# Optimization experiments

Hardware: AMD Instinct MI355X
Metric: run time of the kernel (lower is better)

The kernel has to match this reference:

```python
import jax, jax.numpy as jnp
import numpy as np
from jax import lax


def _conv1x1(x, w):
    # x: [B,Cin,H,W], w: [Cout,Cin]
    return jnp.einsum('bchw,oc->bohw', x, w)


def _dwconv(x, w, pad):
    # depthwise conv, w: [C,1,k,k]
    return lax.conv_general_dilated(
        x, w, window_strides=(1, 1), padding=[(pad, pad), (pad, pad)],
        dimension_numbers=('NCHW', 'OIHW', 'NCHW'),
        feature_group_count=w.shape[0])


def _l2norm(x, axis=-1, eps=1e-12):
    n = jnp.sqrt(jnp.sum(x * x, axis=axis, keepdims=True))
    return x / jnp.maximum(n, eps)


def _topk_masked_softmax(attn, k):
    # attn: [B,H,C,C]; keep top-k per row, -inf elsewhere, softmax
    B, H, C, _ = attn.shape
    flat = attn.reshape(B * H * C, C)
    vals, idx = lax.top_k(flat, k)
    rows = jnp.arange(flat.shape[0])[:, None]
    scat = jnp.full_like(flat, -jnp.inf).at[rows, idx].set(vals)
    return jax.nn.softmax(scat, axis=-1).reshape(B, H, C, C)


def setup_inputs() -> dict:
    key = jax.random.key(0)
    ks = jax.random.split(key, 7)
    dim, heads = 384, 8
    x = jax.random.normal(ks[0], (2, dim, 128, 128), jnp.float32)
    s = 0.02
    w_qkv = jax.random.normal(ks[1], (dim * 3, dim), jnp.float32) * s
    w_dw3 = jax.random.normal(ks[2], (dim * 3, 1, 3, 3), jnp.float32) * s
    w_dw5 = jax.random.normal(ks[3], (dim * 3, 1, 5, 5), jnp.float32) * s
    w_dw7 = jax.random.normal(ks[4], (dim * 3, 1, 7, 7), jnp.float32) * s
    w_pconv = jax.random.normal(ks[5], (dim * 3, dim * 9), jnp.float32) * s
    w_proj = jax.random.normal(ks[6], (dim, dim), jnp.float32) * s
    temperature = jnp.ones((heads, 1, 1), jnp.float32)
    attn_scales = jnp.full((3,), 0.2, jnp.float32)
    return {"x": x, "w_qkv": w_qkv, "w_dw3": w_dw3, "w_dw5": w_dw5,
            "w_dw7": w_dw7, "w_pconv": w_pconv, "w_proj": w_proj,
            "temperature": temperature, "attn_scales": attn_scales}


def reference(x, w_qkv, w_dw3, w_dw5, w_dw7, w_pconv, w_proj, temperature, attn_scales):
    b, c, h, w = x.shape
    heads = temperature.shape[0]
    base = _conv1x1(x, w_qkv)                       # [B,3C,H,W]
    qkv = jnp.concatenate([_dwconv(base, w_dw3, 1),
                           _dwconv(base, w_dw5, 2),
                           _dwconv(base, w_dw7, 3)], axis=1)  # [B,9C,H,W]
    qkv = _conv1x1(qkv, w_pconv)                    # [B,3C,H,W]
    q, k, v = jnp.split(qkv, 3, axis=1)
    def heads_split(t):
        return t.reshape(b, heads, c // heads, h * w)
    q, k, v = heads_split(q), heads_split(k), heads_split(v)
    q = _l2norm(q)
    k = _l2norm(k)
    attn = jnp.einsum('bhcn,bhdn->bhcd', q, k) * temperature  # [B,H,C,C]
    C = q.shape[2]
    out = jnp.zeros_like(v)
    for i, top_k in enumerate([int(C / 2), int(C * 2 / 3), int(C * 3 / 4)]):
        a = _topk_masked_softmax(attn, top_k)
        out = out + attn_scales[i] * jnp.einsum('bhcd,bhdn->bhcn', a, v)
    out = out.reshape(b, c, h, w)
    return _conv1x1(out, w_proj)
```

## Files before the change

kernel.cpp:

```cpp
#include <hip/hip_runtime.h>
#include <hip/hip_bf16.h>
#include <stdint.h>

typedef __attribute__((ext_vector_type(4))) float f32x4;
typedef __attribute__((ext_vector_type(8))) short s16x8;
typedef __attribute__((ext_vector_type(4))) short s16x4;
typedef __attribute__((ext_vector_type(8))) _Float16 f16x8;

__device__ __forceinline__ float bf2f(unsigned short u){
  union { unsigned int i; float f; } v; v.i = ((unsigned int)u) << 16; return v.f;
}
__device__ __forceinline__ unsigned short f2bf(float f){
  union { float f; unsigned int i; } v; v.f = f;
  unsigned int r = v.i + 0x7fffu + ((v.i >> 16) & 1u);
  return (unsigned short)(r >> 16);
}
__device__ __forceinline__ unsigned short f2h(float f){
  union { _Float16 h; unsigned short u; } v; v.h = (_Float16)f; return v.u;
}
__device__ __forceinline__ void gload_lds16(const void* g, void* l){
  __builtin_amdgcn_global_load_lds(
      (const __attribute__((address_space(1))) void*)g,
      (__attribute__((address_space(3))) void*)l, 16, 0, 0);
}

__device__ __forceinline__ void swz_decode(int id, int mtiles, int& m0, int& n0){
  const int xcd = id & 7;
  const int r = id >> 3;
  m0 = (r % mtiles) * 128;
  n0 = ((r / mtiles)*8 + xcd) * 128;
}

template<int MODE>
__global__ __launch_bounds__(256, 2)
void k_gemm(const unsigned short* __restrict__ A, const unsigned short* __restrict__ Bt,
            void* __restrict__ Cp, int M, int N, int K, int ldb){
  __shared__ unsigned short sm[16384];
  const int tid = threadIdx.x;
  const int lane = tid & 63;
  const int wid = tid >> 6;
  int m0, n0;
  swz_decode(blockIdx.x, M >> 7, m0, n0);
  const int wm = wid & 1;
  const int wn = wid >> 1;

  f32x4 acc[4][4];
  #pragma unroll
  for (int i = 0; i < 4; ++i)
    #pragma unroll
    for (int j = 0; j < 4; ++j)
      acc[i][j] = (f32x4){0.f, 0.f, 0.f, 0.f};

  const unsigned short* ga[4];
  const unsigned short* gb[4];
  unsigned short* la[4];
  unsigned short* lb[4];
  #pragma unroll
  for (int i = 0; i < 4; ++i){
    const int row = (wid*4 + i)*8 + (lane >> 3);
    const int slot = (lane & 7) ^ (row & 7);
    ga[i] = A  + (size_t)(m0 + row)*K   + slot*8;
    gb[i] = Bt + (size_t)(n0 + row)*ldb + slot*8;
    la[i] = &sm[(wid*4 + i)*512];
    lb[i] = &sm[8192 + (wid*4 + i)*512];
  }

  const int nkt = K >> 6;
  for (int kt = 0; kt < nkt; ++kt){
    if (kt) __syncthreads();
    #pragma unroll
    for (int i = 0; i < 4; ++i){
      gload_lds16(ga[i] + kt*64, la[i]);
      gload_lds16(gb[i] + kt*64, lb[i]);
    }
    __syncthreads();
    #pragma unroll
    for (int kk = 0; kk < 2; ++kk){
      s16x8 af[4], bfv[4];
      #pragma unroll
      for (int im = 0; im < 4; ++im){
        const int row = wm*64 + im*16 + (lane & 15);
        const int s = ((kk*4) | (lane >> 4)) ^ (row & 7);
        af[im] = *(const s16x8*)((const char*)sm + row*128 + s*16);
      }
      #pragma unroll
      for (int in = 0; in < 4; ++in){
        const int row = wn*64 + in*16 + (lane & 15);
        const int s = ((kk*4) | (lane >> 4)) ^ (row & 7);
        bfv[in] = *(const s16x8*)((const char*)sm + 16384 + row*128 + s*16);
      }
      #pragma unroll
      for (int im = 0; im < 4; ++im)
        #pragma unroll
        for (int in = 0; in < 4; ++in)
          acc[im][in] = __builtin_amdgcn_mfma_f32_16x16x32_bf16(af[im], bfv[in], acc[im][in], 0, 0, 0);
    }
  }

  float* C = (float*)Cp;
  #pragma unroll
  for (int im = 0; im < 4; ++im){
    const int m = m0 + wm*64 + im*16 + (lane >> 4)*4;
    #pragma unroll
    for (int in = 0; in < 4; ++in){
      const int n = n0 + wn*64 + in*16 + (lane & 15);
      #pragma unroll
      for (int r = 0; r < 4; ++r)
        C[(size_t)(m + r)*N + n] = acc[im][in][r];
    }
  }
}

__global__ __launch_bounds__(256, 3)
void k_gemm4w(const unsigned short* __restrict__ A, const unsigned short* __restrict__ Bt,
              float* __restrict__ C){
  __shared__ unsigned short sm[22528];
  const int tid = threadIdx.x;
  const int lane = tid & 63;
  const int wid = tid >> 6;
  const int xcd = blockIdx.x & 7;
  const int rr = blockIdx.x >> 3;
  const int m0 = (rr % 12) * 96;
  const int n0 = ((rr/12)*8 + xcd) * 256;
  const int wm = wid & 1;
  const int wn = wid >> 1;

  f32x4 acc[3][8];
  #pragma unroll
  for (int i = 0; i < 3; ++i)
    #pragma unroll
    for (int j = 0; j < 8; ++j)
      acc[i][j] = (f32x4){0.f, 0.f, 0.f, 0.f};

  const unsigned short* ga[3];
  unsigned short* la[3];
  const unsigned short* gb[8];
  unsigned short* lb[8];
  #pragma unroll
  for (int i = 0; i < 3; ++i){
    const int row = (wid*3 + i)*8 + (lane >> 3);
    const int slot = (lane & 7) ^ (row & 7);
    ga[i] = A + (size_t)(m0 + row)*1152 + slot*8;
    la[i] = &sm[(wid*3 + i)*512];
  }
  #pragma unroll
  for (int i = 0; i < 8; ++i){
    const int row = (wid*8 + i)*8 + (lane >> 3);
    const int slot = (lane & 7) ^ (row & 7);
    gb[i] = Bt + (size_t)(n0 + row)*1152 + slot*8;
    lb[i] = &sm[6144 + (wid*8 + i)*512];
  }

  for (int kt = 0; kt < 18; ++kt){
    if (kt) __syncthreads();
    #pragma unroll
    for (int i = 0; i < 3; ++i)
      gload_lds16(ga[i] + kt*64, la[i]);
    #pragma unroll
    for (int i = 0; i < 8; ++i)
      gload_lds16(gb[i] + kt*64, lb[i]);
    __syncthreads();
    #pragma unroll
    for (int kk = 0; kk < 2; ++kk){
      s16x8 af[3], bfv[8];
      #pragma unroll
      for (int im = 0; im < 3; ++im){
        const int row = wm*48 + im*16 + (lane & 15);
        const int s = ((kk*4) | (lane >> 4)) ^ (row & 7);
        af[im] = *(const s16x8*)((const char*)sm + row*128 + s*16);
      }
      #pragma unroll
      for (int in = 0; in < 8; ++in){
        const int row = wn*128 + in*16 + (lane & 15);
        const int s = ((kk*4) | (lane >> 4)) ^ (row & 7);
        bfv[in] = *(const s16x8*)((const char*)sm + 12288 + row*128 + s*16);
      }
      #pragma unroll
      for (int im = 0; im < 3; ++im)
        #pragma unroll
        for (int in = 0; in < 8; ++in)
          acc[im][in] = __builtin_amdgcn_mfma_f32_16x16x32_bf16(af[im], bfv[in], acc[im][in], 0, 0, 0);
    }
  }

  float* ep = (float*)sm;
  for (int p = 0; p < 4; ++p){
    __syncthreads();
    if (wn == (p >> 1)){
      #pragma unroll
      for (int in2 = 0; in2 < 4; ++in2){
        const int n2 = in2*16 + (lane & 15);
        const int e = (n2 & 7) << 2;
        #pragma unroll
        for (int im = 0; im < 3; ++im){
          const int t = (wm*48 + im*16 + (lane >> 4)*4) >> 2;
          *(f32x4*)(&ep[n2*128 + ((t ^ e) << 2)]) = acc[im][(p & 1)*4 + in2];
        }
      }
    }
    __syncthreads();
    #pragma unroll
    for (int j = 0; j < 6; ++j){
      const int cidx = tid + j*256;
      const int n2 = cidx / 24, t = cidx % 24;
      const int e = (n2 & 7) << 2;
      const f32x4 v = *(const f32x4*)(&ep[n2*128 + ((t ^ e) << 2)]);
      const int cb = (m0 >> 4) + (t >> 2);
      const int off = (t & 3)*4;
      float* dst = C + ((size_t)cb*16384 + (n0 + p*64 + n2))*16 + off;
      *(f32x4*)dst = v;
    }
  }
}

__global__ __launch_bounds__(256, 3)
void k_gemm_f9(const unsigned short* __restrict__ Wp16, const unsigned short* __restrict__ Bt,
               float* __restrict__ qkT, unsigned short* __restrict__ vT, int startPx, int cpx){
  __shared__ unsigned short sm[22528];
  const int tid = threadIdx.x;
  const int lane = tid & 63;
  const int wid = tid >> 6;
  const int xcd = blockIdx.x & 7;
  const int rr = blockIdx.x >> 3;
  const int m0 = (rr % 12) * 96;
  const int n0 = ((rr/12)*8 + xcd) * 256;
  const bool isV = (m0 >= 768);
  const int wm = wid & 1;
  const int wn = wid >> 1;

  f32x4 acc[3][8];
  #pragma unroll
  for (int i = 0; i < 3; ++i)
    #pragma unroll
    for (int j = 0; j < 8; ++j)
      acc[i][j] = (f32x4){0.f, 0.f, 0.f, 0.f};

  const unsigned short* ga[3];
  unsigned short* la[3];
  const unsigned short* gb[8];
  unsigned short* lb[8];
  #pragma unroll
  for (int i = 0; i < 3; ++i){
    const int row = (wid*3 + i)*8 + (lane >> 3);
    const int slot = (lane & 7) ^ (row & 7);
    ga[i] = Wp16 + (size_t)(m0 + row)*3456 + slot*8;
    la[i] = &sm[(wid*3 + i)*512];
  }
  #pragma unroll
  for (int i = 0; i < 8; ++i){
    const int row = (wid*8 + i)*8 + (lane >> 3);
    const int slot = (lane & 7) ^ (row & 7);
    gb[i] = Bt + (size_t)(n0 + row)*3456 + slot*8;
    lb[i] = &sm[6144 + (wid*8 + i)*512];
  }

  for (int kt = 0; kt < 54; ++kt){
    if (kt) __syncthreads();
    #pragma unroll
    for (int i = 0; i < 3; ++i)
      gload_lds16(ga[i] + kt*64, la[i]);
    #pragma unroll
    for (int i = 0; i < 8; ++i)
      gload_lds16(gb[i] + kt*64, lb[i]);
    __syncthreads();
    #pragma unroll
    for (int kk = 0; kk < 2; ++kk){
      f16x8 af[3], bfv[8];
      #pragma unroll
      for (int im = 0; im < 3; ++im){
        const int row = wm*48 + im*16 + (lane & 15);
        const int s = ((kk*4) | (lane >> 4)) ^ (row & 7);
        af[im] = *(const f16x8*)((const char*)sm + row*128 + s*16);
      }
      #pragma unroll
      for (int in = 0; in < 8; ++in){
        const int row = wn*128 + in*16 + (lane & 15);
        const int s = ((kk*4) | (lane >> 4)) ^ (row & 7);
        bfv[in] = *(const f16x8*)((const char*)sm + 12288 + row*128 + s*16);
      }
      #pragma unroll
      for (int im = 0; im < 3; ++im)
        #pragma unroll
        for (int in = 0; in < 8; ++in)
          acc[im][in] = __builtin_amdgcn_mfma_f32_16x16x32_f16(af[im], bfv[in], acc[im][in], 0, 0, 0);
    }
  }

  float* ep = (float*)sm;
  for (int p = 0; p < 4; ++p){
    __syncthreads();
    if (wn == (p >> 1)){
      #pragma unroll
      for (int in2 = 0; in2 < 4; ++in2){
        const int n2 = in2*16 + (lane & 15);
        const int e = (n2 & 7) << 2;
        #pragma unroll
        for (int im = 0; im < 3; ++im){
          const int t = (wm*48 + im*16 + (lane >> 4)*4) >> 2;
          *(f32x4*)(&ep[n2*128 + ((t ^ e) << 2)]) = acc[im][(p & 1)*4 + in2];
        }
      }
    }
    __syncthreads();
    if (!isV){
      #pragma unroll
      for (int j = 0; j < 6; ++j){
        const int cidx = tid + j*256;
        const int n2 = cidx / 24, t = cidx % 24;
        const int e = (n2 & 7) << 2;
        const f32x4 v = *(const f32x4*)(&ep[n2*128 + ((t ^ e) << 2)]);
        *(f32x4*)(qkT + (size_t)(n0 + p*64 + n2)*768 + m0 + t*4) = v;
      }
    } else {
      #pragma unroll
      for (int j = 0; j < 3; ++j){
        const int cidx = tid + j*256;
        const int n2 = cidx / 12, u2 = cidx % 12;
        const int e = (n2 & 7) << 2;
        const f32x4 lo = *(const f32x4*)(&ep[n2*128 + (((2*u2    ) ^ e) << 2)]);
        const f32x4 hi = *(const f32x4*)(&ep[n2*128 + (((2*u2 + 1) ^ e) << 2)]);
        s16x8 o;
        #pragma unroll
        for (int q = 0; q < 4; ++q){ o[q] = (short)f2bf(lo[q]); o[4 + q] = (short)f2bf(hi[q]); }
        *(s16x8*)(vT + (size_t)(startPx + n0 + p*64 + n2)*384 + (m0 - 768) + u2*8) = o;
      }
    }
  }
}

__global__ __launch_bounds__(256)
void k_transpose_xhl(const float* __restrict__ x, unsigned short* __restrict__ xT2){
  __shared__ float lds[64*65];
  const int tid = threadIdx.x;
  const int px0 = blockIdx.x*64;
  const int c0 = blockIdx.y*64;
  #pragma unroll
  for (int it = 0; it < 4; ++it){
    const int idx = tid + it*256;
    const int cl = idx >> 4, col = idx & 15;
    const f32x4 v = *(const f32x4*)(x + (size_t)(c0 + cl)*16384 + px0 + col*4);
    float* d = &lds[cl*65 + col*4];
    d[0] = v[0]; d[1] = v[1]; d[2] = v[2]; d[3] = v[3];
  }
  __syncthreads();
  #pragma unroll
  for (int it = 0; it < 2; ++it){
    const int idx = tid + it*256;
    const int pl = idx >> 3, cg = idx & 7;
    s16x8 h, l;
    #pragma unroll
    for (int j = 0; j < 8; ++j){
      const float v = lds[(cg*8 + j)*65 + pl];
      const unsigned short hb = f2bf(v);
      h[j] = (short)hb;
      l[j] = (short)f2bf(v - bf2f(hb));
    }
    unsigned short* o = xT2 + (size_t)(px0 + pl)*1152 + c0 + cg*8;
    *(s16x8*)(o)       = h;
    *(s16x8*)(o + 384) = l;
    *(s16x8*)(o + 768) = h;
  }
}

__global__ __launch_bounds__(512, 1)
void k_dwconv(const float* __restrict__ base2,
              const float* __restrict__ w3, const float* __restrict__ w5,
              const float* __restrict__ w7, unsigned short* __restrict__ dwT2,
              int y_base_rows, int start_px, int cpx){
  __shared__ float tile[10*72*16];
  __shared__ float wl[16*83];
  const int tid = threadIdx.x;
  const int cb = blockIdx.x;
  const int c0 = cb*16;
  const int y0 = y_base_rows + blockIdx.y*4;
  const int x0 = blockIdx.z*64;

  for (int u = tid; u < 16*83; u += 512){
    float wv;
    if (u < 144){ const int tap = u >> 4, cl = u & 15; wv = w3[(c0 + cl)*9 + tap]; }
    else if (u < 544){ const int v2 = u - 144; const int tap = v2/16, cl = v2%16; wv = w5[(c0 + cl)*25 + tap]; }
    else { const int v2 = u - 544; const int tap = v2/16, cl = v2%16; wv = w7[(c0 + cl)*49 + tap]; }
    wl[u] = wv;
  }
  const float* bb = base2 + (size_t)cb*16384*16;
  for (int u = tid; u < 2880; u += 512){
    const int r = u / 288;
    const int rem = u % 288;
    const int xig = rem >> 2;
    const int cq = rem & 3;
    const int y = y0 + r - 3;
    const int xg = x0 + xig - 3;
    f32x4 v = {0.f,0.f,0.f,0.f};
    if ((unsigned)y < 128u && (unsigned)xg < 128u)
      v = *(const f32x4*)(bb + (size_t)(y*128 + xg)*16 + cq*4);
    *(f32x4*)(&tile[(r*72 + xig)*16 + cq*4]) = v;
  }
  __syncthreads();

  const int cq = tid & 3;
  const int xl = (tid >> 2) & 63;
  const int rh = tid >> 8;
  const float* w3t = wl;
  const float* w5t = wl + 144;
  const float* w7t = wl + 544;

  f32x4 a3[2], a5[2], a7[2];
  #pragma unroll
  for (int r = 0; r < 2; ++r){
    a3[r] = (f32x4){0.f,0.f,0.f,0.f};
    a5[r] = (f32x4){0.f,0.f,0.f,0.f};
    a7[r] = (f32x4){0.f,0.f,0.f,0.f};
  }
  #pragma unroll
  for (int dy = 0; dy < 7; ++dy){
    #pragma unroll
    for (int dx = 0; dx < 7; ++dx){
      const f32x4 w7v = *(const f32x4*)(&w7t[(dy*7 + dx)*16 + cq*4]);
      const bool in5 = (dy >= 1 && dy <= 5 && dx >= 1 && dx <= 5);
      const bool in3 = (dy >= 2 && dy <= 4 && dx >= 2 && dx <= 4);
      f32x4 w5v = {0.f,0.f,0.f,0.f}, w3v = {0.f,0.f,0.f,0.f};
      if (in5) w5v = *(const f32x4*)(&w5t[((dy - 1)*5 + (dx - 1))*16 + cq*4]);
      if (in3) w3v = *(const f32x4*)(&w3t[((dy - 2)*3 + (dx - 2))*16 + cq*4]);
      #pragma unroll
      for (int r = 0; r < 2; ++r){
        const f32x4 f = *(const f32x4*)(&tile[((rh*2 + r + dy)*72 + (xl + dx))*16 + cq*4]);
        a7[r] += f*w7v;
        if (in5) a5[r] += f*w5v;
        if (in3) a3[r] += f*w3v;
      }
    }
  }

  #pragma unroll
  for (int r = 0; r < 2; ++r){
    const int p = (y0 + rh*2 + r)*128 + x0 + xl;
    unsigned short* ob = dwT2 + (size_t)(p - start_px)*3456 + cb*48 + cq*4;
    s16x4 h3, h5, h7;
    #pragma unroll
    for (int j = 0; j < 4; ++j){
      h3[j] = (short)f2h(a3[r][j]);
      h5[j] = (short)f2h(a5[r][j]);
      h7[j] = (short)f2h(a7[r][j]);
    }
    *(s16x4*)(ob)      = h3;
    *(s16x4*)(ob + 16) = h5;
    *(s16x4*)(ob + 32) = h7;
  }
}

__global__ __launch_bounds__(256, 2)
void k_attn_partial2(const float* __restrict__ qkT, float* __restrict__ part, int slotBase){
  __shared__ float qk[16*772];
  const int tid = threadIdx.x;
  const int slot = blockIdx.x;
  const int c0 = tid & 15;
  const int d0 = tid >> 4;

  float acc[8][3][3];
  #pragma unroll
  for (int h = 0; h < 8; ++h)
    #pragma unroll
    for (int i = 0; i < 3; ++i)
      #pragma unroll
      for (int j = 0; j < 3; ++j)
        acc[h][i][j] = 0.f;
  float ssq0 = 0.f, ssq1 = 0.f, ssq2 = 0.f;
  const int ch = tid*3;

  for (int sub = 0; sub < 4; ++sub){
    __syncthreads();
    const int pb = slot*64 + sub*16;
    #pragma unroll
    for (int it = 0; it < 12; ++it){
      const int idx = tid + it*256;
      const int px = idx / 192, s = idx % 192;
      *(f32x4*)(&qk[px*772 + s*4]) = *(const f32x4*)(qkT + (size_t)(pb + px)*768 + s*4);
    }
    __syncthreads();
    for (int px = 0; px < 16; ++px){
      const float* row = &qk[px*772];
      #pragma unroll
      for (int h = 0; h < 8; ++h){
        const float q0 = row[h*48 + c0*3 + 0];
        const float q1 = row[h*48 + c0*3 + 1];
        const float q2 = row[h*48 + c0*3 + 2];
        const float k0 = row[384 + h*48 + d0*3 + 0];
        const float k1 = row[384 + h*48 + d0*3 + 1];
        const float k2 = row[384 + h*48 + d0*3 + 2];
        acc[h][0][0] += q0*k0; acc[h][0][1] += q0*k1; acc[h][0][2] += q0*k2;
        acc[h][1][0] += q1*k0; acc[h][1][1] += q1*k1; acc[h][1][2] += q1*k2;
        acc[h][2][0] += q2*k0; acc[h][2][1] += q2*k1; acc[h][2][2] += q2*k2;
      }
      ssq0 += row[ch]*row[ch];
      ssq1 += row[ch + 1]*row[ch + 1];
      ssq2 += row[ch + 2]*row[ch + 2];
    }
  }

  #pragma unroll
  for (int h = 0; h < 8; ++h){
    float* pp = part + ((size_t)h*256 + slotBase + slot)*2400;
    #pragma unroll
    for (int i = 0; i < 3; ++i)
      #pragma unroll
      for (int j = 0; j < 3; ++j)
        pp[(c0*3 + i)*48 + d0*3 + j] = acc[h][i][j];
  }
  {
    const int hh = (ch < 384) ? (ch / 48) : ((ch - 384) / 48);
    const int cc = (ch < 384) ? (ch % 48) : (48 + ((ch - 384) % 48));
    float* pp = part + ((size_t)hh*256 + slotBase + slot)*2400 + 2304 + cc;
    pp[0] = ssq0; pp[1] = ssq1; pp[2] = ssq2;
  }
}

__global__ __launch_bounds__(256)
void k_attn_combine(const float* __restrict__ part, const float* __restrict__ temp,
                    const float* __restrict__ scales, float* __restrict__ Acomb){
  __shared__ float att[288];
  const int tid = threadIdx.x;
  const int rg = blockIdx.x;
  const int h = blockIdx.y;
  const int r0 = rg*4;
  for (int u = tid; u < 288; u += 256){
    const int off = (u < 192) ? ((r0 + u/48)*48 + (u % 48)) : (2304 + (u - 192));
    float s = 0.f;
    const float* pb = part + (size_t)h*256*2400 + off;
    for (int c2 = 0; c2 < 256; ++c2) s += pb[c2*2400];
    att[u] = s;
  }
  __syncthreads();
  const int w = tid >> 6;
  const int lane = tid & 63;
  const int c = r0 + w;
  const int d = lane;
  const float tmp = temp[h];
  float v;
  if (d < 48){
    const float nq = fmaxf(sqrtf(att[192 + c]), 1e-12f);
    const float nk = fmaxf(sqrtf(att[240 + d]), 1e-12f);
    v = att[w*48 + d] / (nq*nk) * tmp;
  } else v = -3.0e38f;
  float m = v;
  #pragma unroll
  for (int s = 32; s; s >>= 1) m = fmaxf(m, __shfl_xor(m, s, 64));
  int rk = 0;
  for (int l = 0; l < 48; ++l){
    const float vl = __shfl(v, l, 64);
    rk += ((vl > v) || (vl == v && l < d)) ? 1 : 0;
  }
  const float e = (d < 48) ? expf(v - m) : 0.f;
  float e0 = (rk < 24) ? e : 0.f;
  float e1 = (rk < 32) ? e : 0.f;
  float e2 = (rk < 36) ? e : 0.f;
  #pragma unroll
  for (int s = 32; s; s >>= 1){
    e0 += __shfl_xor(e0, s, 64);
    e1 += __shfl_xor(e1, s, 64);
    e2 += __shfl_xor(e2, s, 64);
  }
  const float wgt = e*(((rk < 24) ? scales[0]/e0 : 0.f)
                     + ((rk < 32) ? scales[1]/e1 : 0.f)
                     + ((rk < 36) ? scales[2]/e2 : 0.f));
  if (d < 48) Acomb[((size_t)h*48 + c)*48 + d] = wgt;
}

__global__ __launch_bounds__(256, 2)
void k_av(const unsigned short* __restrict__ vT, const float* __restrict__ Acomb,
          unsigned short* __restrict__ outT){
  __shared__ float As[48*49];
  __shared__ float vs[64*48];
  const int tid = threadIdx.x;
  const int pc = blockIdx.x;
  const int h = blockIdx.y;
  for (int u = tid; u < 2304; u += 256)
    As[(u/48)*49 + (u%48)] = Acomb[(size_t)h*2304 + u];
  const int q = tid & 3;
  const int pl = tid >> 2;
  for (int st = 0; st < 4; ++st){
    __syncthreads();
    const int pb = pc*256 + st*64;
    #pragma unroll
    for (int it = 0; it < 2; ++it){
      const int u = tid + it*256;
      if (u < 384){
        const int p = u / 6, sg = u % 6;
        const s16x8 v8 = *(const s16x8*)(vT + (size_t)(pb + p)*384 + h*48 + sg*8);
        float* d = &vs[p*48 + sg*8];
        #pragma unroll
        for (int j = 0; j < 8; ++j) d[j] = bf2f((unsigned short)v8[j]);
      }
    }
    __syncthreads();
    float a[12];
    #pragma unroll
    for (int i = 0; i < 12; ++i) a[i] = 0.f;
    for (int d = 0; d < 48; ++d){
      const float vv = vs[pl*48 + d];
      #pragma unroll
      for (int i = 0; i < 12; ++i) a[i] += As[(q*12 + i)*49 + d]*vv;
    }
    unsigned short* ob = outT + (size_t)(pb + pl)*384 + h*48 + q*12;
    #pragma unroll
    for (int g = 0; g < 3; ++g){
      s16x4 o;
      #pragma unroll
      for (int j = 0; j < 4; ++j) o[j] = (short)f2bf(a[g*4 + j]);
      *(s16x4*)(ob + g*4) = o;
    }
  }
}

__global__ __launch_bounds__(256)
void k_f32_to_bf16(const float* __restrict__ in, unsigned short* __restrict__ out, int n4){
  const int i = blockIdx.x*256 + threadIdx.x;
  if (i < n4){
    const f32x4 v = *(const f32x4*)(in + (size_t)i*4);
    s16x4 o;
    #pragma unroll
    for (int j = 0; j < 4; ++j) o[j] = (short)f2bf(v[j]);
    *(s16x4*)(out + (size_t)i*4) = o;
  }
}
__global__ __launch_bounds__(256)
void k_prep_wqkv(const float* __restrict__ w, unsigned short* __restrict__ A){
  const int i = blockIdx.x*256 + threadIdx.x;
  const int o = i / 384, c = i % 384;
  const float v = w[i];
  const unsigned short hi = f2bf(v);
  const unsigned short lo = f2bf(v - bf2f(hi));
  unsigned short* r = A + (size_t)o*1152;
  r[c] = hi; r[384 + c] = hi; r[768 + c] = lo;
}
__global__ __launch_bounds__(256)
void k_prep_wp16(const float* __restrict__ w, unsigned short* __restrict__ wp16){
  const int i = blockIdx.x*256 + threadIdx.x;
  const int o = i / 3456, k3 = i % 3456;
  const int cbl = k3 / 48, r2 = k3 % 48, br = r2 / 16, cl = r2 % 16;
  wp16[(size_t)o*3456 + k3] = f2h(w[(size_t)o*3456 + br*1152 + cbl*16 + cl]);
}

extern "C" void kernel_launch(void* const* d_in, const int* in_sizes, int n_in,
                              void* d_out, int out_size, void* d_ws, size_t ws_size,
                              hipStream_t stream){
  const float* x         = (const float*)d_in[0];
  const float* w_qkv     = (const float*)d_in[1];
  const float* w_dw3     = (const float*)d_in[2];
  const float* w_dw5     = (const float*)d_in[3];
  const float* w_dw7     = (const float*)d_in[4];
  const float* w_pconv   = (const float*)d_in[5];
  const float* w_proj    = (const float*)d_in[6];
  const float* temperature = (const float*)d_in[7];
  const float* attn_scales = (const float*)d_in[8];
  float* out = (float*)d_out;
  char* ws = (char*)d_ws;
  const size_t MiB = (size_t)1 << 20;

  unsigned short* Aqkv  = (unsigned short*)(ws);
  unsigned short* Wp16  = (unsigned short*)(ws + 3*MiB);
  unsigned short* Wproj = (unsigned short*)(ws + 11*MiB);
  unsigned short* vT    = (unsigned short*)(ws + 12*MiB);
  char* tailp = ws + (ws_size - 33*MiB);
  float*          part  = (float*)tailp;
  float*          Acomb = (float*)(tailp + 20*MiB);
  unsigned short* outT  = (unsigned short*)(tailp + 21*MiB);

  float*          base2;
  float*          qkTc;
  unsigned short* dwT2;
  unsigned short* xT2;
  int units;
  if (ws_size >= 237*MiB){
    base2 = (float*)(ws + 24*MiB);
    qkTc  = (float*)(ws + 24*MiB);
    dwT2  = (unsigned short*)(ws + 96*MiB);
    xT2   = (unsigned short*)(ws + 96*MiB);
    units = 16;
  } else {
    base2 = (float*)(ws + 24*MiB);
    long long avail = (long long)ws_size - (long long)(96 + 33)*MiB;
    units = (int)(avail / (1024LL*768*4 + 1024LL*3456*2));
    if (units > 16) units = 16;
    units &= ~1;
    if (units < 2) units = 2;
    qkTc = (float*)(ws + 96*MiB);
    dwT2 = (unsigned short*)(ws + 96*MiB + (size_t)units*3*MiB);
    xT2  = (unsigned short*)(ws + 96*MiB);
  }

  k_prep_wqkv<<<dim3(1728), dim3(256), 0, stream>>>(w_qkv, Aqkv);
  k_prep_wp16<<<dim3(15552), dim3(256), 0, stream>>>(w_pconv, Wp16);
  k_f32_to_bf16<<<dim3(144), dim3(256), 0, stream>>>(w_proj, Wproj, 36864);

  for (int b = 0; b < 2; ++b){
    const float* xb = x + (size_t)b*384*16384;
    float* outb = out + (size_t)b*384*16384;
    k_transpose_xhl<<<dim3(256, 6), dim3(256), 0, stream>>>(xb, xT2);
    k_gemm4w<<<dim3(768), dim3(256), 0, stream>>>(Aqkv, xT2, base2);
    for (int u0 = 0; u0 < 16; u0 += units){
      const int cu = (units < 16 - u0) ? units : (16 - u0);
      const int start = u0*1024, cpx = cu*1024;
      k_dwconv<<<dim3(72, cu*2, 2), dim3(512), 0, stream>>>(base2, w_dw3, w_dw5, w_dw7,
                                                            dwT2, start/128, start, cpx);
      k_gemm_f9<<<dim3((cpx/256)*12), dim3(256), 0, stream>>>(Wp16, dwT2, qkTc, vT, start, cpx);
      k_attn_partial2<<<dim3(cpx/64), dim3(256), 0, stream>>>(qkTc, part, start/64);
    }
    k_attn_combine<<<dim3(12, 8), dim3(256), 0, stream>>>(part, temperature, attn_scales, Acomb);
    k_av<<<dim3(64, 8), dim3(256), 0, stream>>>(vT, Acomb, outT);
    k_gemm<2><<<dim3(128*3), dim3(256), 0, stream>>>(Wproj, outT, outb, 384, 16384, 384, 384);
  }
  (void)in_sizes; (void)n_in; (void)out_size; (void)ws_size;
}
```

Before: 867.6 us.

## Fold attention and projection into a fused weight applied directly to dwconv output

When the workspace is large enough, the V rows of the pointwise conv are no longer computed. Instead, the combined attention matrix is multiplied into the V part of the pointwise weights, then by the projection weights, giving a 384x3456 fused weight. One final GEMM over the dwconv output replaces the V GEMM, the attention-times-V kernel and the projection GEMM. This cuts the large GEMM work, at the cost of a K=3456 final GEMM plus small weight-prep kernels and extra fp16/bf16 rounding of the fused weight.

```diff
diff --git a/kernel.cpp b/kernel.cpp
--- a/kernel.cpp
+++ b/kernel.cpp
@@ -17,6 +17,9 @@
 }
 __device__ __forceinline__ unsigned short f2h(float f){
   union { _Float16 h; unsigned short u; } v; v.h = (_Float16)f; return v.u;
+}
+__device__ __forceinline__ float h2f(unsigned short u){
+  union { unsigned short s; _Float16 h; } v; v.s = u; return (float)v.h;
 }
 __device__ __forceinline__ void gload_lds16(const void* g, void* l){
   __builtin_amdgcn_global_load_lds(
@@ -107,6 +110,83 @@
       #pragma unroll
       for (int r = 0; r < 4; ++r)
         C[(size_t)(m + r)*N + n] = acc[im][in][r];
+    }
+  }
+}
+
+__global__ __launch_bounds__(256, 2)
+void k_gemm_small(const unsigned short* __restrict__ A, const unsigned short* __restrict__ Bt,
+                  unsigned short* __restrict__ C){
+  __shared__ unsigned short sm[16384];
+  const int tid = threadIdx.x;
+  const int lane = tid & 63;
+  const int wid = tid >> 6;
+  const int n0 = blockIdx.x * 128;
+  const int m0 = blockIdx.y * 128;
+  const int wm = wid & 1;
+  const int wn = wid >> 1;
+
+  f32x4 acc[4][4];
+  #pragma unroll
+  for (int i = 0; i < 4; ++i)
+    #pragma unroll
+    for (int j = 0; j < 4; ++j)
+      acc[i][j] = (f32x4){0.f, 0.f, 0.f, 0.f};
+
+  const unsigned short* ga[4];
+  const unsigned short* gb[4];
+  unsigned short* la[4];
+  unsigned short* lb[4];
+  #pragma unroll
+  for (int i = 0; i < 4; ++i){
+    const int row = (wid*4 + i)*8 + (lane >> 3);
+    const int slot = (lane & 7) ^ (row & 7);
+    ga[i] = A  + (size_t)(m0 + row)*384 + slot*8;
+    gb[i] = Bt + (size_t)(n0 + row)*384 + slot*8;
+    la[i] = &sm[(wid*4 + i)*512];
+    lb[i] = &sm[8192 + (wid*4 + i)*512];
+  }
+
+  for (int kt = 0; kt < 6; ++kt){
+    if (kt) __syncthreads();
+    #pragma unroll
+    for (int i = 0; i < 4; ++i){
+      gload_lds16(ga[i] + kt*64, la[i]);
+      gload_lds16(gb[i] + kt*64, lb[i]);
+    }
+    __syncthreads();
+    #pragma unroll
+    for (int kk = 0; kk < 2; ++kk){
+      s16x8 af[4], bfv[4];
+      #pragma unroll
+      for (int im = 0; im < 4; ++im){
+        const int row = wm*64 + im*16 + (lane & 15);
+        const int s = ((kk*4) | (lane >> 4)) ^ (row & 7);
+        af[im] = *(const s16x8*)((const char*)sm + row*128 + s*16);
+      }
+      #pragma unroll
+      for (int in = 0; in < 4; ++in){
+        const int row = wn*64 + in*16 + (lane & 15);
+        const int s = ((kk*4) | (lane >> 4)) ^ (row & 7);
+        bfv[in] = *(const s16x8*)((const char*)sm + 16384 + row*128 + s*16);
+      }
+      #pragma unroll
+      for (int im = 0; im < 4; ++im)
+        #pragma unroll
+        for (int in = 0; in < 4; ++in)
+          acc[im][in] = __builtin_amdgcn_mfma_f32_16x16x32_bf16(af[im], bfv[in], acc[im][in], 0, 0, 0);
+    }
+  }
+
+  #pragma unroll
+  for (int im = 0; im < 4; ++im){
+    const int m = m0 + wm*64 + im*16 + (lane >> 4)*4;
+    #pragma unroll
+    for (int in = 0; in < 4; ++in){
+      const int n = n0 + wn*64 + in*16 + (lane & 15);
+      #pragma unroll
+      for (int r = 0; r < 4; ++r)
+        C[(size_t)(m + r)*3456 + n] = f2h(acc[im][in][r]);
     }
   }
 }
@@ -210,6 +290,214 @@
       float* dst = C + ((size_t)cb*16384 + (n0 + p*64 + n2))*16 + off;
       *(f32x4*)dst = v;
     }
+  }
+}
+
+__global__ __launch_bounds__(256, 3)
+void k_gemm_f9qk(const unsigned short* __restrict__ Wp16, const unsigned short* __restrict__ Bt,
+                 float* __restrict__ qkT, int cpx){
+  __shared__ unsigned short sm[22528];
+  const int tid = threadIdx.x;
+  const int lane = tid & 63;
+  const int wid = tid >> 6;
+  const int xcd = blockIdx.x & 7;
+  const int rr = blockIdx.x >> 3;
+  const int m0 = (rr % 8) * 96;
+  const int n0 = ((rr/8)*8 + xcd) * 256;
+  const int wm = wid & 1;
+  const int wn = wid >> 1;
+
+  f32x4 acc[3][8];
+  #pragma unroll
+  for (int i = 0; i < 3; ++i)
+    #pragma unroll
+    for (int j = 0; j < 8; ++j)
+      acc[i][j] = (f32x4){0.f, 0.f, 0.f, 0.f};
+
+  const unsigned short* ga[3];
+  unsigned short* la[3];
+  const unsigned short* gb[8];
+  unsigned short* lb[8];
+  #pragma unroll
+  for (int i = 0; i < 3; ++i){
+    const int row = (wid*3 + i)*8 + (lane >> 3);
+    const int slot = (lane & 7) ^ (row & 7);
+    ga[i] = Wp16 + (size_t)(m0 + row)*3456 + slot*8;
+    la[i] = &sm[(wid*3 + i)*512];
+  }
+  #pragma unroll
+  for (int i = 0; i < 8; ++i){
+    const int row = (wid*8 + i)*8 + (lane >> 3);
+    const int slot = (lane & 7) ^ (row & 7);
+    gb[i] = Bt + (size_t)(n0 + row)*3456 + slot*8;
+    lb[i] = &sm[6144 + (wid*8 + i)*512];
+  }
+
+  for (int kt = 0; kt < 54; ++kt){
+    if (kt) __syncthreads();
+    #pragma unroll
+    for (int i = 0; i < 3; ++i)
+      gload_lds16(ga[i] + kt*64, la[i]);
+    #pragma unroll
+    for (int i = 0; i < 8; ++i)
+      gload_lds16(gb[i] + kt*64, lb[i]);
+    __syncthreads();
+    #pragma unroll
+    for (int kk = 0; kk < 2; ++kk){
+      f16x8 af[3], bfv[8];
+      #pragma unroll
+      for (int im = 0; im < 3; ++im){
+        const int row = wm*48 + im*16 + (lane & 15);
+        const int s = ((kk*4) | (lane >> 4)) ^ (row & 7);
+        af[im] = *(const f16x8*)((const char*)sm + row*128 + s*16);
+      }
+      #pragma unroll
+      for (int in = 0; in < 8; ++in){
+        const int row = wn*128 + in*16 + (lane & 15);
+        const int s = ((kk*4) | (lane >> 4)) ^ (row & 7);
+        bfv[in] = *(const f16x8*)((const char*)sm + 12288 + row*128 + s*16);
+      }
+      #pragma unroll
+      for (int im = 0; im < 3; ++im)
+        #pragma unroll
+        for (int in = 0; in < 8; ++in)
+          acc[im][in] = __builtin_amdgcn_mfma_f32_16x16x32_f16(af[im], bfv[in], acc[im][in], 0, 0, 0);
+    }
+  }
+
+  float* ep = (float*)sm;
+  for (int p = 0; p < 4; ++p){
+    __syncthreads();
+    if (wn == (p >> 1)){
+      #pragma unroll
+      for (int in2 = 0; in2 < 4; ++in2){
+        const int n2 = in2*16 + (lane & 15);
+        const int e = (n2 & 7) << 2;
+        #pragma unroll
+        for (int im = 0; im < 3; ++im){
+          const int t = (wm*48 + im*16 + (lane >> 4)*4) >> 2;
+          *(f32x4*)(&ep[n2*128 + ((t ^ e) << 2)]) = acc[im][(p & 1)*4 + in2];
+        }
+      }
+    }
+    __syncthreads();
+    #pragma unroll
+    for (int j = 0; j < 6; ++j){
+      const int cidx = tid + j*256;
+      const int n2 = cidx / 24, t = cidx % 24;
+      const int e = (n2 & 7) << 2;
+      const f32x4 v = *(const f32x4*)(&ep[n2*128 + ((t ^ e) << 2)]);
+      *(f32x4*)(qkT + (size_t)(n0 + p*64 + n2)*768 + m0 + t*4) = v;
+    }
+  }
+}
+
+__global__ __launch_bounds__(256, 3)
+void k_gemm_fin(const unsigned short* __restrict__ Wf16, const unsigned short* __restrict__ Bt,
+                float* __restrict__ C, int cpx){
+  __shared__ unsigned short sm[22528];
+  const int tid = threadIdx.x;
+  const int lane = tid & 63;
+  const int wid = tid >> 6;
+  const int xcd = blockIdx.x & 7;
+  const int rr = blockIdx.x >> 3;
+  const int m0 = (rr % 4) * 96;
+  const int n0 = ((rr/4)*8 + xcd) * 256;
+  const int wm = wid & 1;
+  const int wn = wid >> 1;
+
+  f32x4 acc[3][8];
+  #pragma unroll
+  for (int i = 0; i < 3; ++i)
+    #pragma unroll
+    for (int j = 0; j < 8; ++j)
+      acc[i][j] = (f32x4){0.f, 0.f, 0.f, 0.f};
+
+  const unsigned short* ga[3];
+  unsigned short* la[3];
+  const unsigned short* gb[8];
+  unsigned short* lb[8];
+  #pragma unroll
+  for (int i = 0; i < 3; ++i){
+    const int row = (wid*3 + i)*8 + (lane >> 3);
+    const int slot = (lane & 7) ^ (row & 7);
+    ga[i] = Wf16 + (size_t)(m0 + row)*3456 + slot*8;
+    la[i] = &sm[(wid*3 + i)*512];
+  }
+  #pragma unroll
+  for (int i = 0; i < 8; ++i){
+    const int row = (wid*8 + i)*8 + (lane >> 3);
+    const int slot = (lane & 7) ^ (row & 7);
+    gb[i] = Bt + (size_t)(n0 + row)*3456 + slot*8;
+    lb[i] = &sm[6144 + (wid*8 + i)*512];
+  }
+
+  for (int kt = 0; kt < 54; ++kt){
+    if (kt) __syncthreads();
+    #pragma unroll
+    for (int i = 0; i < 3; ++i)
+      gload_lds16(ga[i] + kt*64, la[i]);
+    #pragma unroll
+    for (int i = 0; i < 8; ++i)
+      gload_lds16(gb[i] + kt*64, lb[i]);
+    __syncthreads();
+    #pragma unroll
+    for (int kk = 0; kk < 2; ++kk){
+      f16x8 af[3], bfv[8];
+      #pragma unroll
+      for (int im = 0; im < 3; ++im){
+        const int row = wm*48 + im*16 + (lane & 15);
+        const int s = ((kk*4) | (lane >> 4)) ^ (row & 7);
+        af[im] = *(const f16x8*)((const char*)sm + row*128 + s*16);
+      }
+      #pragma unroll
+      for (int in = 0; in < 8; ++in){
+        const int row = wn*128 + in*16 + (lane & 15);
+        const int s = ((kk*4) | (lane >> 4)) ^ (row & 7);
+        bfv[in] = *(const f16x8*)((const char*)sm + 12288 + row*128 + s*16);
+      }
+      #pragma unroll
+      for (int im = 0; im < 3; ++im)
+        #pragma unroll
+        for (int in = 0; in < 8; ++in)
+          acc[im][in] = __builtin_amdgcn_mfma_f32_16x16x32_f16(af[im], bfv[in], acc[im][in], 0, 0, 0);
+    }
+  }
+
+  #pragma unroll
+  for (int im = 0; im < 3; ++im){
+    const int m = m0 + wm*48 + im*16 + (lane >> 4)*4;
+    #pragma unroll
+    for (int in = 0; in < 8; ++in){
+      const int n = n0 + wn*128 + in*16 + (lane & 15);
+      #pragma unroll
+      for (int r = 0; r < 4; ++r)
+        C[(size_t)(m + r)*16384 + n] = acc[im][in][r];
+    }
+  }
+}
+
+__global__ __launch_bounds__(256)
+void k_awv(const float* __restrict__ Acomb, const unsigned short* __restrict__ Wp16,
+           unsigned short* __restrict__ awvT){
+  __shared__ float a[2304];
+  __shared__ unsigned short wv[6144];
+  const int tid = threadIdx.x;
+  const int h = blockIdx.x;
+  const int k0 = blockIdx.y * 128;
+  for (int u = tid; u < 2304; u += 256) a[u] = Acomb[(size_t)h*2304 + u];
+  for (int u = tid; u < 6144; u += 256){
+    const int d = u >> 7, j = u & 127;
+    wv[u] = Wp16[(size_t)(768 + h*48 + d)*3456 + k0 + j];
+  }
+  __syncthreads();
+  for (int u = tid; u < 6144; u += 256){
+    const int j = u / 48, c = u % 48;
+    float s = 0.f;
+    #pragma unroll
+    for (int d = 0; d < 48; ++d)
+      s += a[c*48 + d] * h2f(wv[d*128 + j]);
+    awvT[(size_t)(k0 + j)*384 + h*48 + c] = f2bf(s);
   }
 }
 
@@ -663,14 +951,17 @@
   char* tailp = ws + (ws_size - 33*MiB);
   float*          part  = (float*)tailp;
   float*          Acomb = (float*)(tailp + 20*MiB);
-  unsigned short* outT  = (unsigned short*)(tailp + 21*MiB);
+  unsigned short* awvT  = (unsigned short*)(tailp + 21*MiB);
+  unsigned short* Wf16  = (unsigned short*)(tailp + 24*MiB);
+  unsigned short* outT  = (unsigned short*)(tailp + 27*MiB - 6*MiB);
 
   float*          base2;
   float*          qkTc;
   unsigned short* dwT2;
   unsigned short* xT2;
   int units;
-  if (ws_size >= 237*MiB){
+  const bool single = (ws_size >= 237*MiB);
+  if (single){
     base2 = (float*)(ws + 24*MiB);
     qkTc  = (float*)(ws + 24*MiB);
     dwT2  = (unsigned short*)(ws + 96*MiB);
@@ -697,17 +988,29 @@
     float* outb = out + (size_t)b*384*16384;
     k_transpose_xhl<<<dim3(256, 6), dim3(256), 0, stream>>>(xb, xT2);
     k_gemm4w<<<dim3(768), dim3(256), 0, stream>>>(Aqkv, xT2, base2);
-    for (int u0 = 0; u0 < 16; u0 += units){
-      const int cu = (units < 16 - u0) ? units : (16 - u0);
-      const int start = u0*1024, cpx = cu*1024;
-      k_dwconv<<<dim3(72, cu*2, 2), dim3(512), 0, stream>>>(base2, w_dw3, w_dw5, w_dw7,
-                                                            dwT2, start/128, start, cpx);
-      k_gemm_f9<<<dim3((cpx/256)*12), dim3(256), 0, stream>>>(Wp16, dwT2, qkTc, vT, start, cpx);
-      k_attn_partial2<<<dim3(cpx/64), dim3(256), 0, stream>>>(qkTc, part, start/64);
-    }
-    k_attn_combine<<<dim3(12, 8), dim3(256), 0, stream>>>(part, temperature, attn_scales, Acomb);
-    k_av<<<dim3(64, 8), dim3(256), 0, stream>>>(vT, Acomb, outT);
-    k_gemm<2><<<dim3(128*3), dim3(256), 0, stream>>>(Wproj, outT, outb, 384, 16384, 384, 384);
+    if (single){
+      const int cpx = 16384;
+      k_dwconv<<<dim3(72, 32, 2), dim3(512), 0, stream>>>(base2, w_dw3, w_dw5, w_dw7,
+                                                          dwT2, 0, 0, cpx);
+      k_gemm_f9qk<<<dim3((cpx/256)*8), dim3(256), 0, stream>>>(Wp16, dwT2, qkTc, cpx);
+      k_attn_partial2<<<dim3(cpx/64), dim3(256), 0, stream>>>(qkTc, part, 0);
+      k_attn_combine<<<dim3(12, 8), dim3(256), 0, stream>>>(part, temperature, attn_scales, Acomb);
+      k_awv<<<dim3(8, 27), dim3(256), 0, stream>>>(Acomb, Wp16, awvT);
+      k_gemm_small<<<dim3(27, 3), dim3(256), 0, stream>>>(Wproj, awvT, Wf16);
+      k_gemm_fin<<<dim3((cpx/256)*4), dim3(256), 0, stream>>>(Wf16, dwT2, outb, cpx);
+    } else {
+      for (int u0 = 0; u0 < 16; u0 += units){
+        const int cu = (units < 16 - u0) ? units : (16 - u0);
+        const int start = u0*1024, cpx = cu*1024;
+        k_dwconv<<<dim3(72, cu*2, 2), dim3(512), 0, stream>>>(base2, w_dw3, w_dw5, w_dw7,
+                                                              dwT2, start/128, start, cpx);
+        k_gemm_f9<<<dim3((cpx/256)*12), dim3(256), 0, stream>>>(Wp16, dwT2, qkTc, vT, start, cpx);
+        k_attn_partial2<<<dim3(cpx/64), dim3(256), 0, stream>>>(qkTc, part, start/64);
+      }
+      k_attn_combine<<<dim3(12, 8), dim3(256), 0, stream>>>(part, temperature, attn_scales, Acomb);
+      k_av<<<dim3(64, 8), dim3(256), 0, stream>>>(vT, Acomb, outT);
+      k_gemm<2><<<dim3(128*3), dim3(256), 0, stream>>>(Wproj, outT, outb, 384, 16384, 384, 384);
+    }
   }
   (void)in_sizes; (void)n_in; (void)out_size; (void)ws_size;
 }
```

Result: slower. 985.4 us (+13.6%).
